# Performance work log

Measured on AMD Instinct MI355X. Metric: run time of the kernel, lower is better.

The kernel has to match this reference:

```python
import jax, jax.numpy as jnp
import numpy as np

N_IN, N_OUT, N_TO = 64, 64, 16  # connection table: each output plane gets N_TO random input planes
K = N_OUT * N_TO                # 1024 connections
KH, KW = 3, 3
B, H, W = 4, 192, 192


def setup_inputs() -> dict:
    key = jax.random.key(0)
    kx, kw_, kb, kc = jax.random.split(key, 4)
    x = jax.random.normal(kx, (B, N_IN, H, W), dtype=jnp.float32)
    weight = jax.random.normal(kw_, (K, KH, KW), dtype=jnp.float32) * (1.0 / np.sqrt(KH * KW * N_TO))
    bias = jax.random.normal(kb, (N_OUT,), dtype=jnp.float32) * 0.01
    # maps.random semantics: each output plane j has exactly N_TO input connections
    conn_in = jax.random.randint(kc, (K,), 0, N_IN, dtype=jnp.int32)
    conn_out = jnp.repeat(jnp.arange(N_OUT, dtype=jnp.int32), N_TO)
    return {"x": x, "weight": weight, "bias": bias, "conn_in": conn_in, "conn_out": conn_out}


def reference(x, weight, bias, conn_in, conn_out):
    # x: [B, nIn, H, W]; weight: [K, kH, kW]; connection k convolves plane conn_in[k]
    # into plane conn_out[k] with its own kernel (valid conv, stride 1).
    nK = weight.shape[0]
    nOut = bias.shape[0]
    xg = x[:, conn_in]                       # [B, K, H, W] gather input planes per connection
    y = jax.lax.conv_general_dilated(
        xg, weight[:, None],                 # kernel [K, 1, kH, kW], grouped => per-connection conv
        window_strides=(1, 1), padding='VALID',
        feature_group_count=nK,
        dimension_numbers=('NCHW', 'OIHW', 'NCHW'))  # [B, K, Ho, Wo]
    # scatter-add connections into their output planes
    out = jax.ops.segment_sum(jnp.moveaxis(y, 1, 0), conn_out, num_segments=nOut)  # [nOut, B, Ho, Wo]
    return jnp.moveaxis(out, 0, 1) + bias[None, :, None, None]
```

## Files before the change

kernel.cpp:

```cpp
#include <hip/hip_runtime.h>
#include <hip/hip_bf16.h>

#define HH 192
#define WW 192
#define HOUT 190
#define NCH 64
#define W2_N (64 * 9 * 64)

typedef __attribute__((ext_vector_type(8))) short bf16x8;
typedef __attribute__((ext_vector_type(4))) float f32x4;

static __device__ __forceinline__ ushort f2bf(float f) {
    __hip_bfloat16 h = __float2bfloat16(f);
    return *reinterpret_cast<ushort*>(&h);
}
static __device__ __forceinline__ uint pack2bf(float lo, float hi) {
    return (uint)f2bf(lo) | ((uint)f2bf(hi) << 16);
}

__global__ __launch_bounds__(256) void build_w2(const float* __restrict__ w,
                                                const int* __restrict__ conn,
                                                ushort* __restrict__ w2) {
    int idx = blockIdx.x * 256 + threadIdx.x;
    if (idx >= W2_N) return;
    int o = idx / 576, rem = idx - o * 576, tap = rem >> 6, c = rem & 63;
    float s = 0.f;
    #pragma unroll
    for (int t = 0; t < 16; ++t) {
        int k = o * 16 + t;
        if (conn[k] == c) s += w[k * 9 + tap];
    }
    w2[idx] = f2bf(s);
}

__global__ __launch_bounds__(256, 3) void scm_mfma(
    const float* __restrict__ x,
    const ushort* __restrict__ w2,
    const float* __restrict__ bias,
    float* __restrict__ out)
{
    __shared__ ushort xt[10 * 18 * 72];

    const int tid  = threadIdx.x;
    const int lane = tid & 63;
    const int wv   = tid >> 6;
    const int col  = lane & 15;
    const int g    = lane >> 4;

    const int bid = blockIdx.x;
    const int lid = (bid & 7) * 144 + (bid >> 3);
    const int b      = lid / 288;
    const int tileid = lid % 288;
    const int ti0 = (tileid / 12) * 8;
    const int tj0 = (tileid % 12) * 16;

    {
        const int srr  = lane / 18;
        const int scol = lane - srr * 18;
        const bool act = lane < 54;
        int gc = tj0 + scol; if (gc > 191) gc = 191;
        int gr0 = ti0 + srr;     if (gr0 > 191) gr0 = 191;
        int gr1 = ti0 + srr + 3; if (gr1 > 191) gr1 = 191;
        int gr2 = ti0 + srr + 6; if (gr2 > 191) gr2 = 191;
        int gr3 = ti0 + srr + 9; if (gr3 > 191) gr3 = 191;

        #pragma unroll
        for (int pass = 0; pass < 2; ++pass) {
            float v[8][4];
            #pragma unroll
            for (int pj = 0; pj < 8; ++pj) {
                const int c = wv * 16 + pass * 8 + pj;
                const float* xc = x + ((size_t)(b * NCH + c)) * (HH * WW);
                v[pj][0] = xc[gr0 * WW + gc];
                v[pj][1] = xc[gr1 * WW + gc];
                v[pj][2] = xc[gr2 * WW + gc];
                v[pj][3] = xc[gr3 * WW + gc];
            }
            __builtin_amdgcn_sched_barrier(0);
            if (act) {
                #pragma unroll
                for (int pp = 0; pp < 4; ++pp) {
                    const int c = wv * 16 + pass * 8 + 2 * pp;
                    uint k0 = pack2bf(v[2 * pp][0], v[2 * pp + 1][0]);
                    uint k1 = pack2bf(v[2 * pp][1], v[2 * pp + 1][1]);
                    uint k2 = pack2bf(v[2 * pp][2], v[2 * pp + 1][2]);
                    uint k3 = pack2bf(v[2 * pp][3], v[2 * pp + 1][3]);
                    *(uint*)&xt[((srr    ) * 18 + scol) * 72 + c] = k0;
                    *(uint*)&xt[((srr + 3) * 18 + scol) * 72 + c] = k1;
                    *(uint*)&xt[((srr + 6) * 18 + scol) * 72 + c] = k2;
                    if (srr == 0)
                        *(uint*)&xt[(9 * 18 + scol) * 72 + c] = k3;
                }
            }
        }
    }
    __syncthreads();

    f32x4 acc[8];
    #pragma unroll
    for (int i = 0; i < 8; ++i) acc[i] = (f32x4){0.f, 0.f, 0.f, 0.f};

    const ushort* ap0 = &xt[col * 72 + g * 8];
    const ushort* bp  = w2 + (16 * wv + col) * 576 + g * 8;

    #pragma unroll
    for (int s = 0; s < 2; ++s) {
        bf16x8 Bs[9];
        #pragma unroll
        for (int tap = 0; tap < 9; ++tap)
            Bs[tap] = *(const bf16x8*)(bp + tap * 64 + s * 32);
        #pragma unroll
        for (int kw = 0; kw < 3; ++kw) {
            bf16x8 f[10];
            #pragma unroll
            for (int R = 0; R < 10; ++R)
                f[R] = *(const bf16x8*)(ap0 + (R * 18 + kw) * 72 + s * 32);
            __builtin_amdgcn_sched_barrier(0);
            #pragma unroll
            for (int Mt = 0; Mt < 8; ++Mt) {
                acc[Mt] = __builtin_amdgcn_mfma_f32_16x16x32_bf16(Bs[kw],     f[Mt],     acc[Mt], 0, 0, 0);
                acc[Mt] = __builtin_amdgcn_mfma_f32_16x16x32_bf16(Bs[3 + kw], f[Mt + 1], acc[Mt], 0, 0, 0);
                acc[Mt] = __builtin_amdgcn_mfma_f32_16x16x32_bf16(Bs[6 + kw], f[Mt + 2], acc[Mt], 0, 0, 0);
            }
        }
    }

    const int pcol = tj0 + col;
    const int obase = 16 * wv + 4 * g;
    float bv[4];
    #pragma unroll
    for (int reg = 0; reg < 4; ++reg) bv[reg] = bias[obase + reg];

    if (pcol < HOUT) {
        #pragma unroll
        for (int Mt = 0; Mt < 8; ++Mt) {
            const int row = ti0 + Mt;
            if (row < HOUT) {
                float* rp = out + ((size_t)(b * NCH + obase) * HOUT + row) * HOUT + pcol;
                #pragma unroll
                for (int reg = 0; reg < 4; ++reg)
                    rp[(size_t)reg * HOUT * HOUT] = acc[Mt][reg] + bv[reg];
            }
        }
    }
}

extern "C" void kernel_launch(void* const* d_in, const int* in_sizes, int n_in,
                              void* d_out, int out_size, void* d_ws, size_t ws_size,
                              hipStream_t stream) {
    const float* x       = (const float*)d_in[0];
    const float* weight  = (const float*)d_in[1];
    const float* bias    = (const float*)d_in[2];
    const int*   conn_in = (const int*)d_in[3];

    ushort* w2 = (ushort*)d_ws;

    build_w2<<<dim3((W2_N + 255) / 256), dim3(256), 0, stream>>>(weight, conn_in, w2);

    scm_mfma<<<dim3(1152), dim3(256), 0, stream>>>(x, w2, bias, (float*)d_out);
}
```

Baseline: 34.55 us.

## Pre-transpose input to NHWC bf16 and load MFMA operands from global

Adds a separate kernel that casts x to bf16 and transposes it to NHWC in workspace. The main kernel then drops its LDS staging tile and reads MFMA B-fragments directly from global/L2 with contiguous 16-byte loads. This is meant to remove the scattered fp32 gathers and the LDS round trip, but it adds an extra kernel launch plus a full write and reread of a bf16 copy of x.

```diff
diff --git a/kernel.cpp b/kernel.cpp
--- a/kernel.cpp
+++ b/kernel.cpp
@@ -6,6 +6,7 @@
 #define HOUT 190
 #define NCH 64
 #define W2_N (64 * 9 * 64)
+#define XG_OFF 131072
 
 typedef __attribute__((ext_vector_type(8))) short bf16x8;
 typedef __attribute__((ext_vector_type(4))) float f32x4;
@@ -13,9 +14,6 @@
 static __device__ __forceinline__ ushort f2bf(float f) {
     __hip_bfloat16 h = __float2bfloat16(f);
     return *reinterpret_cast<ushort*>(&h);
-}
-static __device__ __forceinline__ uint pack2bf(float lo, float hi) {
-    return (uint)f2bf(lo) | ((uint)f2bf(hi) << 16);
 }
 
 __global__ __launch_bounds__(256) void build_w2(const float* __restrict__ w,
@@ -33,14 +31,37 @@
     w2[idx] = f2bf(s);
 }
 
+__global__ __launch_bounds__(256) void nhwc_cast(const float* __restrict__ x,
+                                                 ushort* __restrict__ xg) {
+    __shared__ ushort t[64][68];
+    const int tid = threadIdx.x;
+    const int seg = blockIdx.x % 3;
+    const int r   = blockIdx.x / 3;
+    const int b   = blockIdx.y;
+
+    const int cc  = tid & 63;
+    const int chq = tid >> 6;
+    #pragma unroll
+    for (int it = 0; it < 16; ++it) {
+        const int ch = it * 4 + chq;
+        t[cc][ch] = f2bf(x[(((size_t)(b * NCH + ch)) * HH + r) * WW + seg * 64 + cc]);
+    }
+    __syncthreads();
+
+    const int c = tid >> 2;
+    const int q = tid & 3;
+    const ushort* src = &t[c][q * 16];
+    ushort* dst = xg + (((size_t)(b * HH + r)) * WW + seg * 64 + c) * NCH + q * 16;
+    *(uint4*)(dst)     = *(const uint4*)(src);
+    *(uint4*)(dst + 8) = *(const uint4*)(src + 8);
+}
+
 __global__ __launch_bounds__(256, 3) void scm_mfma(
-    const float* __restrict__ x,
+    const ushort* __restrict__ xg,
     const ushort* __restrict__ w2,
     const float* __restrict__ bias,
     float* __restrict__ out)
 {
-    __shared__ ushort xt[10 * 18 * 72];
-
     const int tid  = threadIdx.x;
     const int lane = tid & 63;
     const int wv   = tid >> 6;
@@ -54,54 +75,24 @@
     const int ti0 = (tileid / 12) * 8;
     const int tj0 = (tileid % 12) * 16;
 
-    {
-        const int srr  = lane / 18;
-        const int scol = lane - srr * 18;
-        const bool act = lane < 54;
-        int gc = tj0 + scol; if (gc > 191) gc = 191;
-        int gr0 = ti0 + srr;     if (gr0 > 191) gr0 = 191;
-        int gr1 = ti0 + srr + 3; if (gr1 > 191) gr1 = 191;
-        int gr2 = ti0 + srr + 6; if (gr2 > 191) gr2 = 191;
-        int gr3 = ti0 + srr + 9; if (gr3 > 191) gr3 = 191;
-
-        #pragma unroll
-        for (int pass = 0; pass < 2; ++pass) {
-            float v[8][4];
-            #pragma unroll
-            for (int pj = 0; pj < 8; ++pj) {
-                const int c = wv * 16 + pass * 8 + pj;
-                const float* xc = x + ((size_t)(b * NCH + c)) * (HH * WW);
-                v[pj][0] = xc[gr0 * WW + gc];
-                v[pj][1] = xc[gr1 * WW + gc];
-                v[pj][2] = xc[gr2 * WW + gc];
-                v[pj][3] = xc[gr3 * WW + gc];
-            }
-            __builtin_amdgcn_sched_barrier(0);
-            if (act) {
-                #pragma unroll
-                for (int pp = 0; pp < 4; ++pp) {
-                    const int c = wv * 16 + pass * 8 + 2 * pp;
-                    uint k0 = pack2bf(v[2 * pp][0], v[2 * pp + 1][0]);
-                    uint k1 = pack2bf(v[2 * pp][1], v[2 * pp + 1][1]);
-                    uint k2 = pack2bf(v[2 * pp][2], v[2 * pp + 1][2]);
-                    uint k3 = pack2bf(v[2 * pp][3], v[2 * pp + 1][3]);
-                    *(uint*)&xt[((srr    ) * 18 + scol) * 72 + c] = k0;
-                    *(uint*)&xt[((srr + 3) * 18 + scol) * 72 + c] = k1;
-                    *(uint*)&xt[((srr + 6) * 18 + scol) * 72 + c] = k2;
-                    if (srr == 0)
-                        *(uint*)&xt[(9 * 18 + scol) * 72 + c] = k3;
-                }
-            }
-        }
+    int rowoff[10];
+    #pragma unroll
+    for (int R = 0; R < 10; ++R) {
+        int gr = ti0 + R; if (gr > 191) gr = 191;
+        rowoff[R] = (b * HH + gr) * (WW * NCH);
     }
-    __syncthreads();
+    int coloff[3];
+    #pragma unroll
+    for (int kw = 0; kw < 3; ++kw) {
+        int gc = tj0 + col + kw; if (gc > 191) gc = 191;
+        coloff[kw] = gc * NCH + g * 8;
+    }
 
     f32x4 acc[8];
     #pragma unroll
     for (int i = 0; i < 8; ++i) acc[i] = (f32x4){0.f, 0.f, 0.f, 0.f};
 
-    const ushort* ap0 = &xt[col * 72 + g * 8];
-    const ushort* bp  = w2 + (16 * wv + col) * 576 + g * 8;
+    const ushort* bp = w2 + (16 * wv + col) * 576 + g * 8;
 
     #pragma unroll
     for (int s = 0; s < 2; ++s) {
@@ -114,7 +105,7 @@
             bf16x8 f[10];
             #pragma unroll
             for (int R = 0; R < 10; ++R)
-                f[R] = *(const bf16x8*)(ap0 + (R * 18 + kw) * 72 + s * 32);
+                f[R] = *(const bf16x8*)(xg + rowoff[R] + coloff[kw] + s * 32);
             __builtin_amdgcn_sched_barrier(0);
             #pragma unroll
             for (int Mt = 0; Mt < 8; ++Mt) {
@@ -154,8 +145,10 @@
     const int*   conn_in = (const int*)d_in[3];
 
     ushort* w2 = (ushort*)d_ws;
+    ushort* xg = (ushort*)((char*)d_ws + XG_OFF);
 
+    nhwc_cast<<<dim3(3 * HH, 4), dim3(256), 0, stream>>>(x, xg);
     build_w2<<<dim3((W2_N + 255) / 256), dim3(256), 0, stream>>>(weight, conn_in, w2);
 
-    scm_mfma<<<dim3(1152), dim3(256), 0, stream>>>(x, w2, bias, (float*)d_out);
+    scm_mfma<<<dim3(1152), dim3(256), 0, stream>>>(xg, w2, bias, (float*)d_out);
 }
```

New measurement: 68.90 us. +99.4%, slower.
